# Performance work log

Hardware: AMD Instinct MI355X
Metric: run time of the kernel (lower is better)

## Reference

```python
import jax, jax.numpy as jnp
import numpy as np


def setup_inputs() -> dict:
    key = jax.random.key(0)
    k1, k2 = jax.random.split(key)
    Nd, Ld, E = 128, 128, 128   # docs, doc sentences, embed_size
    Nq, Lq = 128, 32            # queries, query sentences
    # ColBERT-style: embeddings are L2-normalized per sentence in embed()
    doc = jax.random.normal(k1, (Nd, Ld, E), dtype=jnp.float32)
    doc = doc / jnp.linalg.norm(doc, axis=-1, keepdims=True)
    # query embeddings are stored transposed: [Nq, E, Lq]
    q = jax.random.normal(k2, (Nq, Lq, E), dtype=jnp.float32)
    q = q / jnp.linalg.norm(q, axis=-1, keepdims=True)
    query = jnp.transpose(q, (0, 2, 1))  # [Nq, E, Lq]
    return {"doc_tokens": doc, "query_tokens": query}


def reference(doc_tokens, query_tokens):
    # max_sim(doc, query, sentence_wise=False, full_mat=True)
    # doc_tokens: [Nd, Ld, E]; query_tokens: [Nq, E, Lq]
    # scores[q,d,t,l] = sum_e doc[d,t,e] * query[q,e,l]   (bmm over cross product)
    scores = jnp.einsum('dte,qel->qdtl', doc_tokens, query_tokens)
    # max over doc tokens t, sum over query tokens l -> [Nq, Nd]
    return jnp.sum(jnp.max(scores, axis=2), axis=-1)
```

## Files before the change

kernel.cpp:

```cpp
#include <hip/hip_runtime.h>
#include <hip/hip_bf16.h>

typedef short short8 __attribute__((ext_vector_type(8)));
typedef float f32x16 __attribute__((ext_vector_type(16)));

#define ND 128
#define LD 128
#define EE 128
#define NQ 128
#define LQ 32
#define DSTRIDE 136

__global__ __launch_bounds__(256)
void convert_kernel(const float* __restrict__ doc, const float* __restrict__ qry,
                    __hip_bfloat16* __restrict__ docA, __hip_bfloat16* __restrict__ qB2) {
  const int tid = threadIdx.x;
  if (blockIdx.x < 128) {
    const int d = blockIdx.x;
    __shared__ __hip_bfloat16 s[LD * DSTRIDE];
    const float4* src = reinterpret_cast<const float4*>(doc + d * LD * EE);
    #pragma unroll
    for (int i = 0; i < 16; ++i) {
      int c = i * 256 + tid;
      int t = c >> 5;
      int e = (c & 31) << 2;
      float4 v = src[c];
      union { ushort4 u; __hip_bfloat16 b[4]; } o;
      o.b[0] = __float2bfloat16(v.x);
      o.b[1] = __float2bfloat16(v.y);
      o.b[2] = __float2bfloat16(v.z);
      o.b[3] = __float2bfloat16(v.w);
      *reinterpret_cast<ushort4*>(&s[t * DSTRIDE + e]) = o.u;
    }
    __syncthreads();
    uint4* dst = reinterpret_cast<uint4*>(docA + d * LD * EE);
    #pragma unroll
    for (int i = 0; i < 8; ++i) {
      int cc = i * 256 + tid;
      int mt = cc >> 9;
      int ks = (cc >> 6) & 7;
      int lo = cc & 63;
      int t  = mt * 32 + (lo & 31);
      int e0 = ks * 16 + (lo >> 5) * 8;
      dst[cc] = *reinterpret_cast<const uint4*>(&s[t * DSTRIDE + e0]);
    }
    return;
  }
  const int q = blockIdx.x - 128;
  __shared__ float sq[EE][LQ + 1];
  const float* src = qry + q * EE * LQ;
  #pragma unroll
  for (int i = 0; i < 4; ++i) {
    int c = i * 256 + tid;
    int e = c >> 3;
    int l = (c & 7) << 2;
    float4 v = reinterpret_cast<const float4*>(src)[c];
    sq[e][l + 0] = v.x;
    sq[e][l + 1] = v.y;
    sq[e][l + 2] = v.z;
    sq[e][l + 3] = v.w;
  }
  __syncthreads();
  uint4* dst = reinterpret_cast<uint4*>(qB2 + q * LQ * EE);
  #pragma unroll
  for (int i = 0; i < 2; ++i) {
    int cc = i * 256 + tid;
    int ks = cc >> 6;
    int lo = cc & 63;
    int l  = lo & 31;
    int e0 = ks * 16 + (lo >> 5) * 8;
    union { uint4 u; __hip_bfloat16 b[8]; } o;
    #pragma unroll
    for (int j = 0; j < 8; ++j)
      o.b[j] = __float2bfloat16(sq[e0 + j][l]);
    dst[cc] = o.u;
  }
}

__global__ __launch_bounds__(256, 2)
void maxsim_kernel(const __hip_bfloat16* __restrict__ docA,
                   const __hip_bfloat16* __restrict__ qB2,
                   float* __restrict__ out) {
  __shared__ float pmax[32][4][32];
  const int d    = blockIdx.x;
  const int qg   = blockIdx.y;
  const int tid  = threadIdx.x;
  const int wave = tid >> 6;
  const int lane = tid & 63;
  const int q0   = qg * 32;

  const short8* As = reinterpret_cast<const short8*>(docA)
                   + (d * 4 + wave) * 512 + lane;
  short8 afrag[8];
  #pragma unroll
  for (int ks = 0; ks < 8; ++ks) afrag[ks] = As[ks * 64];

  const short8* Bs = reinterpret_cast<const short8*>(qB2) + q0 * 512 + lane;

  short8 b[2][2][8];
  #pragma unroll
  for (int ks = 0; ks < 8; ++ks) {
    b[0][0][ks] = Bs[ks * 64];
    b[0][1][ks] = Bs[(8 + ks) * 64];
  }

  #pragma unroll 2
  for (int p = 0; p < 16; ++p) {
    const int cur = p & 1, nxt = cur ^ 1;
    if (p < 15) {
      const short8* Bn = Bs + (2 * p + 2) * 512;
      #pragma unroll
      for (int ks = 0; ks < 8; ++ks) {
        b[nxt][0][ks] = Bn[ks * 64];
        b[nxt][1][ks] = Bn[(8 + ks) * 64];
      }
    }
    f32x16 a0 = {0.f, 0.f, 0.f, 0.f, 0.f, 0.f, 0.f, 0.f,
                 0.f, 0.f, 0.f, 0.f, 0.f, 0.f, 0.f, 0.f};
    f32x16 a1 = a0;
    #pragma unroll
    for (int ks = 0; ks < 8; ++ks) {
      a0 = __builtin_amdgcn_mfma_f32_32x32x16_bf16(afrag[ks], b[cur][0][ks], a0, 0, 0, 0);
      a1 = __builtin_amdgcn_mfma_f32_32x32x16_bf16(afrag[ks], b[cur][1][ks], a1, 0, 0, 0);
    }
    float m0 = fmaxf(
        fmaxf(fmaxf(fmaxf(a0[0], a0[1]), fmaxf(a0[2], a0[3])),
              fmaxf(fmaxf(a0[4], a0[5]), fmaxf(a0[6], a0[7]))),
        fmaxf(fmaxf(fmaxf(a0[8], a0[9]), fmaxf(a0[10], a0[11])),
              fmaxf(fmaxf(a0[12], a0[13]), fmaxf(a0[14], a0[15]))));
    float m1 = fmaxf(
        fmaxf(fmaxf(fmaxf(a1[0], a1[1]), fmaxf(a1[2], a1[3])),
              fmaxf(fmaxf(a1[4], a1[5]), fmaxf(a1[6], a1[7]))),
        fmaxf(fmaxf(fmaxf(a1[8], a1[9]), fmaxf(a1[10], a1[11])),
              fmaxf(fmaxf(a1[12], a1[13]), fmaxf(a1[14], a1[15]))));
    m0 = fmaxf(m0, __shfl_xor(m0, 32, 64));
    m1 = fmaxf(m1, __shfl_xor(m1, 32, 64));
    if (lane < 32) {
      pmax[2 * p    ][wave][lane] = m0;
      pmax[2 * p + 1][wave][lane] = m1;
    }
  }
  __syncthreads();

  {
    int q  = tid >> 3;
    int c0 = (tid & 7) * 4;
    float ssum = 0.f;
    #pragma unroll
    for (int i = 0; i < 4; ++i) {
      int c = c0 + i;
      ssum += fmaxf(fmaxf(pmax[q][0][c], pmax[q][1][c]),
                    fmaxf(pmax[q][2][c], pmax[q][3][c]));
    }
    ssum += __shfl_xor(ssum, 1, 64);
    ssum += __shfl_xor(ssum, 2, 64);
    ssum += __shfl_xor(ssum, 4, 64);
    if ((tid & 7) == 0) out[(q0 + q) * ND + d] = ssum;
  }
}

extern "C" void kernel_launch(void* const* d_in, const int* in_sizes, int n_in,
                              void* d_out, int out_size, void* d_ws, size_t ws_size,
                              hipStream_t stream) {
  const float* doc = (const float*)d_in[0];
  const float* qry = (const float*)d_in[1];
  float* out = (float*)d_out;

  __hip_bfloat16* docA = (__hip_bfloat16*)d_ws;
  __hip_bfloat16* qB2  = docA + ND * LD * EE;

  convert_kernel<<<dim3(256), dim3(256), 0, stream>>>(doc, qry, docA, qB2);
  maxsim_kernel<<<dim3(ND, NQ / 32), dim3(256), 0, stream>>>(docA, qB2, out);
}
```

Before: 83.55 us.

## Give each wave all doc tokens and a subset of queries, drop LDS reduction

```diff
diff --git a/kernel.cpp b/kernel.cpp
--- a/kernel.cpp
+++ b/kernel.cpp
@@ -77,85 +77,79 @@
   }
 }
 
-__global__ __launch_bounds__(256, 2)
+__global__ __launch_bounds__(256)
 void maxsim_kernel(const __hip_bfloat16* __restrict__ docA,
                    const __hip_bfloat16* __restrict__ qB2,
                    float* __restrict__ out) {
-  __shared__ float pmax[32][4][32];
   const int d    = blockIdx.x;
   const int qg   = blockIdx.y;
   const int tid  = threadIdx.x;
   const int wave = tid >> 6;
   const int lane = tid & 63;
-  const int q0   = qg * 32;
+  const int q0   = qg * 32 + wave * 8;
 
-  const short8* As = reinterpret_cast<const short8*>(docA)
-                   + (d * 4 + wave) * 512 + lane;
-  short8 afrag[8];
+  const short8* As = reinterpret_cast<const short8*>(docA) + d * 2048 + lane;
+  short8 afrag[4][8];
   #pragma unroll
-  for (int ks = 0; ks < 8; ++ks) afrag[ks] = As[ks * 64];
+  for (int mt = 0; mt < 4; ++mt)
+    #pragma unroll
+    for (int ks = 0; ks < 8; ++ks)
+      afrag[mt][ks] = As[(mt * 8 + ks) * 64];
 
   const short8* Bs = reinterpret_cast<const short8*>(qB2) + q0 * 512 + lane;
 
-  short8 b[2][2][8];
-  #pragma unroll
-  for (int ks = 0; ks < 8; ++ks) {
-    b[0][0][ks] = Bs[ks * 64];
-    b[0][1][ks] = Bs[(8 + ks) * 64];
-  }
+  #pragma unroll 1
+  for (int p = 0; p < 4; ++p) {
+    const short8* Bp = Bs + p * 1024;
+    short8 b0[8], b1[8];
+    #pragma unroll
+    for (int ks = 0; ks < 8; ++ks) {
+      b0[ks] = Bp[ks * 64];
+      b1[ks] = Bp[(8 + ks) * 64];
+    }
 
-  #pragma unroll 2
-  for (int p = 0; p < 16; ++p) {
-    const int cur = p & 1, nxt = cur ^ 1;
-    if (p < 15) {
-      const short8* Bn = Bs + (2 * p + 2) * 512;
+    float cm0 = -3.0e38f, cm1 = -3.0e38f;
+    #pragma unroll
+    for (int mt = 0; mt < 4; ++mt) {
+      f32x16 a0 = {0.f, 0.f, 0.f, 0.f, 0.f, 0.f, 0.f, 0.f,
+                   0.f, 0.f, 0.f, 0.f, 0.f, 0.f, 0.f, 0.f};
+      f32x16 a1 = a0;
       #pragma unroll
       for (int ks = 0; ks < 8; ++ks) {
-        b[nxt][0][ks] = Bn[ks * 64];
-        b[nxt][1][ks] = Bn[(8 + ks) * 64];
+        a0 = __builtin_amdgcn_mfma_f32_32x32x16_bf16(afrag[mt][ks], b0[ks], a0, 0, 0, 0);
+        a1 = __builtin_amdgcn_mfma_f32_32x32x16_bf16(afrag[mt][ks], b1[ks], a1, 0, 0, 0);
       }
+      float m0 = fmaxf(
+          fmaxf(fmaxf(fmaxf(a0[0], a0[1]), fmaxf(a0[2], a0[3])),
+                fmaxf(fmaxf(a0[4], a0[5]), fmaxf(a0[6], a0[7]))),
+          fmaxf(fmaxf(fmaxf(a0[8], a0[9]), fmaxf(a0[10], a0[11])),
+                fmaxf(fmaxf(a0[12], a0[13]), fmaxf(a0[14], a0[15]))));
+      cm0 = fmaxf(cm0, m0);
+      float m1 = fmaxf(
+          fmaxf(fmaxf(fmaxf(a1[0], a1[1]), fmaxf(a1[2], a1[3])),
+                fmaxf(fmaxf(a1[4], a1[5]), fmaxf(a1[6], a1[7]))),
+          fmaxf(fmaxf(fmaxf(a1[8], a1[9]), fmaxf(a1[10], a1[11])),
+                fmaxf(fmaxf(a1[12], a1[13]), fmaxf(a1[14], a1[15]))));
+      cm1 = fmaxf(cm1, m1);
     }
-    f32x16 a0 = {0.f, 0.f, 0.f, 0.f, 0.f, 0.f, 0.f, 0.f,
-                 0.f, 0.f, 0.f, 0.f, 0.f, 0.f, 0.f, 0.f};
-    f32x16 a1 = a0;
-    #pragma unroll
-    for (int ks = 0; ks < 8; ++ks) {
-      a0 = __builtin_amdgcn_mfma_f32_32x32x16_bf16(afrag[ks], b[cur][0][ks], a0, 0, 0, 0);
-      a1 = __builtin_amdgcn_mfma_f32_32x32x16_bf16(afrag[ks], b[cur][1][ks], a1, 0, 0, 0);
+
+    cm0 = fmaxf(cm0, __shfl_xor(cm0, 32, 64));
+    cm1 = fmaxf(cm1, __shfl_xor(cm1, 32, 64));
+    float s0 = cm0, s1 = cm1;
+    s0 += __shfl_xor(s0, 1, 64);
+    s0 += __shfl_xor(s0, 2, 64);
+    s0 += __shfl_xor(s0, 4, 64);
+    s0 += __shfl_xor(s0, 8, 64);
+    s0 += __shfl_xor(s0, 16, 64);
+    s1 += __shfl_xor(s1, 1, 64);
+    s1 += __shfl_xor(s1, 2, 64);
+    s1 += __shfl_xor(s1, 4, 64);
+    s1 += __shfl_xor(s1, 8, 64);
+    s1 += __shfl_xor(s1, 16, 64);
+    if (lane == 0) {
+      out[(q0 + 2 * p) * ND + d]     = s0;
+      out[(q0 + 2 * p + 1) * ND + d] = s1;
     }
-    float m0 = fmaxf(
-        fmaxf(fmaxf(fmaxf(a0[0], a0[1]), fmaxf(a0[2], a0[3])),
-              fmaxf(fmaxf(a0[4], a0[5]), fmaxf(a0[6], a0[7]))),
-        fmaxf(fmaxf(fmaxf(a0[8], a0[9]), fmaxf(a0[10], a0[11])),
-              fmaxf(fmaxf(a0[12], a0[13]), fmaxf(a0[14], a0[15]))));
-    float m1 = fmaxf(
-        fmaxf(fmaxf(fmaxf(a1[0], a1[1]), fmaxf(a1[2], a1[3])),
-              fmaxf(fmaxf(a1[4], a1[5]), fmaxf(a1[6], a1[7]))),
-        fmaxf(fmaxf(fmaxf(a1[8], a1[9]), fmaxf(a1[10], a1[11])),
-              fmaxf(fmaxf(a1[12], a1[13]), fmaxf(a1[14], a1[15]))));
-    m0 = fmaxf(m0, __shfl_xor(m0, 32, 64));
-    m1 = fmaxf(m1, __shfl_xor(m1, 32, 64));
-    if (lane < 32) {
-      pmax[2 * p    ][wave][lane] = m0;
-      pmax[2 * p + 1][wave][lane] = m1;
-    }
-  }
-  __syncthreads();
-
-  {
-    int q  = tid >> 3;
-    int c0 = (tid & 7) * 4;
-    float ssum = 0.f;
-    #pragma unroll
-    for (int i = 0; i < 4; ++i) {
-      int c = c0 + i;
-      ssum += fmaxf(fmaxf(pmax[q][0][c], pmax[q][1][c]),
-                    fmaxf(pmax[q][2][c], pmax[q][3][c]));
-    }
-    ssum += __shfl_xor(ssum, 1, 64);
-    ssum += __shfl_xor(ssum, 2, 64);
-    ssum += __shfl_xor(ssum, 4, 64);
-    if ((tid & 7) == 0) out[(q0 + q) * ND + d] = ssum;
   }
 }
 
```

New measurement: 77.22 us. -7.6%, faster.
